# Performance work log

Measured on AMD Instinct MI355X. Metric: run time of the kernel, lower is better.

## Reference

```python
import jax, jax.numpy as jnp
import numpy as np

NEG_SLOPE = 0.01  # torch nn.LeakyReLU default


def setup_inputs() -> dict:
    key = jax.random.key(0)
    k1, k2, k3 = jax.random.split(key, 3)
    B, H, D, L = 4, 8, 64, 2048
    q = jax.random.normal(k1, (B, H, D, L), dtype=jnp.float32)
    k = jax.random.normal(k2, (B, H, D, L), dtype=jnp.float32)
    v = jax.random.normal(k3, (B, H, D, L), dtype=jnp.float32)
    return {"q": q, "k": k, "v": v}


def reference(q, k, v):
    # q, k, v: [B, H, D, L] (note: feature dim BEFORE length, as in the torch module)
    d_tensor = q.shape[2]
    scale = 1.0 / np.sqrt(d_tensor).astype(np.float32)
    # scores = LeakyReLU(q^T k / sqrt(d)) : [B, H, Lq, Lk]
    scores = jnp.einsum('bhdq,bhdk->bhqk', q, k) * scale
    scores = jax.nn.leaky_relu(scores, negative_slope=NEG_SLOPE)
    psi = jax.nn.softmax(scores, axis=-1)
    # out = (psi @ v^T)^T : [B, H, D, Lq]
    out = jnp.einsum('bhqk,bhdk->bhdq', psi, v)
    return out
```

## Files before the change

kernel.cpp:

```cpp
#include <hip/hip_runtime.h>
#include <math.h>

#define DD 64
#define LL 2048
#define TQ 128
#define TK 64
#define NTILES (LL / TK)
#define NTHREADS 512
#define NHEADS 32
#define QSCALE 0.18033688011112042f

typedef __bf16 bf16_t;
typedef __bf16 bf16x8 __attribute__((ext_vector_type(8)));
typedef float f32x16 __attribute__((ext_vector_type(16)));

struct __align__(16) SMemA {
  bf16_t Qs[TQ][72];
  bf16_t Ks[TK][72];
  bf16_t Vs[DD][72];
};
union __align__(16) SMemU {
  SMemA a;
  float Oe[TQ][65];
};

__global__ __launch_bounds__(256)
void prep_t(const float* __restrict__ src, bf16_t* __restrict__ dst, float scale) {
  __shared__ bf16_t tile[64][72];
  const int tid  = threadIdx.x;
  const int head = blockIdx.y;
  const int l0   = blockIdx.x * 64;
  const float* sp = src + (size_t)head * DD * LL;
  {
    int d  = tid >> 2;
    int lg = (tid & 3) * 16;
    const float* rp = sp + (size_t)d * LL + l0 + lg;
    for (int g = 0; g < 4; ++g) {
      float4 a = *(const float4*)(rp + 4 * g);
      tile[lg + 4 * g + 0][d] = (bf16_t)(a.x * scale);
      tile[lg + 4 * g + 1][d] = (bf16_t)(a.y * scale);
      tile[lg + 4 * g + 2][d] = (bf16_t)(a.z * scale);
      tile[lg + 4 * g + 3][d] = (bf16_t)(a.w * scale);
    }
  }
  __syncthreads();
  {
    int l  = tid & 63;
    int dh = (tid >> 6) * 16;
    bf16x8 r0 = *(const bf16x8*)&tile[l][dh];
    bf16x8 r1 = *(const bf16x8*)&tile[l][dh + 8];
    bf16_t* op = dst + ((size_t)head * LL + l0 + l) * DD + dh;
    *(bf16x8*)op = r0;
    *(bf16x8*)(op + 8) = r1;
  }
}

__global__ __launch_bounds__(256)
void prep_c(const float* __restrict__ src, bf16_t* __restrict__ dst) {
  size_t i = ((size_t)blockIdx.x * 256 + threadIdx.x) * 8;
  float4 a = *(const float4*)(src + i);
  float4 b = *(const float4*)(src + i + 4);
  bf16x8 p;
  p[0] = (bf16_t)a.x; p[1] = (bf16_t)a.y; p[2] = (bf16_t)a.z; p[3] = (bf16_t)a.w;
  p[4] = (bf16_t)b.x; p[5] = (bf16_t)b.y; p[6] = (bf16_t)b.z; p[7] = (bf16_t)b.w;
  *(bf16x8*)(dst + i) = p;
}

__global__ __launch_bounds__(NTHREADS, 4)
void attn_flash_bf16(const bf16_t* __restrict__ Qt, const bf16_t* __restrict__ Kt,
                     const bf16_t* __restrict__ Vb, float* __restrict__ out) {
  __shared__ SMemU sm;
  __shared__ float rs1[TQ];
  const int tid  = threadIdx.x;
  const int w    = tid >> 6;
  const int lane = tid & 63;
  const int l31  = lane & 31;
  const int hh   = lane >> 5;
  const int strip = w & 3;
  const int half  = w >> 2;
  const int wbase = strip * 32;
  const int lkh   = half * 32;
  const int head = blockIdx.y;
  const int q0   = blockIdx.x * TQ;
  const bf16_t* qp = Qt + (size_t)head * LL * DD;
  const bf16_t* kp = Kt + (size_t)head * LL * DD;
  const bf16_t* vp = Vb + (size_t)head * DD * LL;

  {
    int lq  = tid & 127;
    int d0q = (tid >> 7) * 16;
    const bf16_t* src = qp + (size_t)(q0 + lq) * DD + d0q;
    bf16x8 a0 = *(const bf16x8*)src;
    bf16x8 a1 = *(const bf16x8*)(src + 8);
    *(bf16x8*)&sm.a.Qs[lq][d0q] = a0;
    *(bf16x8*)&sm.a.Qs[lq][d0q + 8] = a1;
  }

  const int klk = tid & 63;
  const int kd0 = (tid >> 6) * 8;
  const int vd  = tid >> 3;
  const int vc8 = (tid & 7) * 8;

  bf16x8 kreg = *(const bf16x8*)(kp + (size_t)klk * DD + kd0);
  bf16x8 vreg = *(const bf16x8*)(vp + (size_t)vd * LL + vc8);

  __syncthreads();
  bf16x8 bq[4];
  for (int kk = 0; kk < 4; ++kk)
    bq[kk] = *(const bf16x8*)&sm.a.Qs[wbase + l31][kk * 16 + 8 * hh];

  f32x16 oacc[2];
  for (int dt = 0; dt < 2; ++dt)
    for (int r = 0; r < 16; ++r) oacc[dt][r] = 0.f;
  float rsum = 0.f;

  for (int t = 0; t < NTILES; ++t) {
    __syncthreads();
    *(bf16x8*)&sm.a.Ks[klk][kd0] = kreg;
    *(bf16x8*)&sm.a.Vs[vd][vc8]  = vreg;
    __syncthreads();

    if (t + 1 < NTILES) {
      const int lk0n = (t + 1) * TK;
      kreg = *(const bf16x8*)(kp + (size_t)(lk0n + klk) * DD + kd0);
      vreg = *(const bf16x8*)(vp + (size_t)vd * LL + lk0n + vc8);
    }

    f32x16 st;
    for (int r = 0; r < 16; ++r) st[r] = 0.f;
    for (int kk = 0; kk < 4; ++kk) {
      bf16x8 ak = *(const bf16x8*)&sm.a.Ks[lkh + l31][kk * 16 + 8 * hh];
      st = __builtin_amdgcn_mfma_f32_32x32x16_bf16(ak, bq[kk], st, 0, 0, 0);
    }

    unsigned pb[8];
    for (int r = 0; r < 16; ++r) {
      float s = st[r];
      s = fmaxf(s, 0.01f * s);
      float p = __builtin_amdgcn_exp2f(s);
      rsum += p;
      st[r] = p;
    }
    for (int qq = 0; qq < 8; ++qq) {
      union { bf16_t b[2]; unsigned u; } pk;
      pk.b[0] = (bf16_t)st[2 * qq];
      pk.b[1] = (bf16_t)st[2 * qq + 1];
      pb[qq] = pk.u;
    }

    for (int kk2 = 0; kk2 < 2; ++kk2) {
      unsigned l0 = pb[4 * kk2 + 0], l1 = pb[4 * kk2 + 1];
      unsigned l2 = pb[4 * kk2 + 2], l3 = pb[4 * kk2 + 3];
      unsigned s0 = hh ? l0 : l2;
      unsigned s1 = hh ? l1 : l3;
      unsigned f0 = (unsigned)__shfl_xor((int)s0, 32);
      unsigned f1 = (unsigned)__shfl_xor((int)s1, 32);
      union { unsigned u[4]; bf16x8 v; } ap;
      ap.u[0] = hh ? f0 : l0;
      ap.u[1] = hh ? f1 : l1;
      ap.u[2] = hh ? l2 : f0;
      ap.u[3] = hh ? l3 : f1;
      const int lkb = lkh + kk2 * 16 + 8 * hh;
      for (int dt = 0; dt < 2; ++dt) {
        bf16x8 bv = *(const bf16x8*)&sm.a.Vs[dt * 32 + l31][lkb];
        oacc[dt] = __builtin_amdgcn_mfma_f32_32x32x16_bf16(ap.v, bv, oacc[dt], 0, 0, 0);
      }
    }
  }

  float rtot = rsum + __shfl_xor(rsum, 32);
  __syncthreads();
  if (half == 1) {
    rs1[wbase + l31] = rtot;
    for (int r = 0; r < 16; ++r) {
      int row = (r & 3) + 8 * (r >> 2) + 4 * hh;
      for (int dt = 0; dt < 2; ++dt)
        sm.Oe[wbase + row][dt * 32 + l31] = oacc[dt][r];
    }
  }
  __syncthreads();
  if (half == 0) {
    float tot = rtot + rs1[wbase + l31];
    rs1[wbase + l31] = 1.0f / tot;
    float inv[16];
    for (int r = 0; r < 16; ++r) {
      int row = (r & 3) + 8 * (r >> 2) + 4 * hh;
      inv[r] = rs1[wbase + row];
    }
    for (int r = 0; r < 16; ++r) {
      int row = (r & 3) + 8 * (r >> 2) + 4 * hh;
      for (int dt = 0; dt < 2; ++dt) {
        int col = dt * 32 + l31;
        sm.Oe[wbase + row][col] = (oacc[dt][r] + sm.Oe[wbase + row][col]) * inv[r];
      }
    }
  }
  __syncthreads();
  float* op = out + (size_t)head * DD * LL + q0;
  for (int i = 0; i < 16; ++i) {
    int idx = tid + NTHREADS * i;
    int d   = idx >> 7;
    int lq  = idx & 127;
    op[(size_t)d * LL + lq] = sm.Oe[lq][d];
  }
}

__global__ __launch_bounds__(NTHREADS, 4)
void attn_flash_fb(const float* __restrict__ q, const float* __restrict__ k,
                   const float* __restrict__ v, float* __restrict__ out) {
  __shared__ SMemU sm;
  __shared__ float rs1[TQ];
  const int tid  = threadIdx.x;
  const int w    = tid >> 6;
  const int lane = tid & 63;
  const int l31  = lane & 31;
  const int hh   = lane >> 5;
  const int strip = w & 3;
  const int half  = w >> 2;
  const int wbase = strip * 32;
  const int lkh   = half * 32;
  const int head = blockIdx.y;
  const int q0   = blockIdx.x * TQ;
  const size_t hoff = (size_t)head * DD * LL;
  const float* qp = q + hoff;
  const float* kp = k + hoff;
  const float* vp = v + hoff;
  {
    int lq  = tid & 127;
    int d0q = (tid >> 7) * 16;
    const float* src = qp + q0 + lq;
    for (int g = 0; g < 2; ++g) {
      bf16x8 pk;
      for (int j = 0; j < 8; ++j)
        pk[j] = (bf16_t)(src[(size_t)(d0q + g * 8 + j) * LL] * QSCALE);
      *(bf16x8*)&sm.a.Qs[lq][d0q + g * 8] = pk;
    }
  }
  const int klk = tid & 63;
  const int kd0 = (tid >> 6) * 8;
  const int vd  = tid >> 3;
  const int vc8 = (tid & 7) * 8;
  float  kreg[8];
  float4 vreg[2];
  {
    const float* ks = kp + klk;
    for (int j = 0; j < 8; ++j) kreg[j] = ks[(size_t)(kd0 + j) * LL];
    vreg[0] = *(const float4*)(vp + (size_t)vd * LL + vc8);
    vreg[1] = *(const float4*)(vp + (size_t)vd * LL + vc8 + 4);
  }
  __syncthreads();
  bf16x8 bq[4];
  for (int kk = 0; kk < 4; ++kk)
    bq[kk] = *(const bf16x8*)&sm.a.Qs[wbase + l31][kk * 16 + 8 * hh];
  f32x16 oacc[2];
  for (int dt = 0; dt < 2; ++dt)
    for (int r = 0; r < 16; ++r) oacc[dt][r] = 0.f;
  float rsum = 0.f;
  for (int t = 0; t < NTILES; ++t) {
    __syncthreads();
    {
      bf16x8 pk;
      for (int j = 0; j < 8; ++j) pk[j] = (bf16_t)kreg[j];
      *(bf16x8*)&sm.a.Ks[klk][kd0] = pk;
      bf16x8 pv;
      pv[0] = (bf16_t)vreg[0].x; pv[1] = (bf16_t)vreg[0].y;
      pv[2] = (bf16_t)vreg[0].z; pv[3] = (bf16_t)vreg[0].w;
      pv[4] = (bf16_t)vreg[1].x; pv[5] = (bf16_t)vreg[1].y;
      pv[6] = (bf16_t)vreg[1].z; pv[7] = (bf16_t)vreg[1].w;
      *(bf16x8*)&sm.a.Vs[vd][vc8] = pv;
    }
    __syncthreads();
    if (t + 1 < NTILES) {
      const int lk0n = (t + 1) * TK;
      const float* ks = kp + lk0n + klk;
      for (int j = 0; j < 8; ++j) kreg[j] = ks[(size_t)(kd0 + j) * LL];
      vreg[0] = *(const float4*)(vp + (size_t)vd * LL + lk0n + vc8);
      vreg[1] = *(const float4*)(vp + (size_t)vd * LL + lk0n + vc8 + 4);
    }
    f32x16 st;
    for (int r = 0; r < 16; ++r) st[r] = 0.f;
    for (int kk = 0; kk < 4; ++kk) {
      bf16x8 ak = *(const bf16x8*)&sm.a.Ks[lkh + l31][kk * 16 + 8 * hh];
      st = __builtin_amdgcn_mfma_f32_32x32x16_bf16(ak, bq[kk], st, 0, 0, 0);
    }
    unsigned pb[8];
    for (int r = 0; r < 16; ++r) {
      float s = st[r];
      s = fmaxf(s, 0.01f * s);
      float p = __builtin_amdgcn_exp2f(s);
      rsum += p;
      st[r] = p;
    }
    for (int qq = 0; qq < 8; ++qq) {
      union { bf16_t b[2]; unsigned u; } pk;
      pk.b[0] = (bf16_t)st[2 * qq];
      pk.b[1] = (bf16_t)st[2 * qq + 1];
      pb[qq] = pk.u;
    }
    for (int kk2 = 0; kk2 < 2; ++kk2) {
      unsigned l0 = pb[4 * kk2 + 0], l1 = pb[4 * kk2 + 1];
      unsigned l2 = pb[4 * kk2 + 2], l3 = pb[4 * kk2 + 3];
      unsigned s0 = hh ? l0 : l2;
      unsigned s1 = hh ? l1 : l3;
      unsigned f0 = (unsigned)__shfl_xor((int)s0, 32);
      unsigned f1 = (unsigned)__shfl_xor((int)s1, 32);
      union { unsigned u[4]; bf16x8 v; } ap;
      ap.u[0] = hh ? f0 : l0;
      ap.u[1] = hh ? f1 : l1;
      ap.u[2] = hh ? l2 : f0;
      ap.u[3] = hh ? l3 : f1;
      const int lkb = lkh + kk2 * 16 + 8 * hh;
      for (int dt = 0; dt < 2; ++dt) {
        bf16x8 bv = *(const bf16x8*)&sm.a.Vs[dt * 32 + l31][lkb];
        oacc[dt] = __builtin_amdgcn_mfma_f32_32x32x16_bf16(ap.v, bv, oacc[dt], 0, 0, 0);
      }
    }
  }
  float rtot = rsum + __shfl_xor(rsum, 32);
  __syncthreads();
  if (half == 1) {
    rs1[wbase + l31] = rtot;
    for (int r = 0; r < 16; ++r) {
      int row = (r & 3) + 8 * (r >> 2) + 4 * hh;
      for (int dt = 0; dt < 2; ++dt)
        sm.Oe[wbase + row][dt * 32 + l31] = oacc[dt][r];
    }
  }
  __syncthreads();
  if (half == 0) {
    float tot = rtot + rs1[wbase + l31];
    rs1[wbase + l31] = 1.0f / tot;
    float inv[16];
    for (int r = 0; r < 16; ++r) {
      int row = (r & 3) + 8 * (r >> 2) + 4 * hh;
      inv[r] = rs1[wbase + row];
    }
    for (int r = 0; r < 16; ++r) {
      int row = (r & 3) + 8 * (r >> 2) + 4 * hh;
      for (int dt = 0; dt < 2; ++dt) {
        int col = dt * 32 + l31;
        sm.Oe[wbase + row][col] = (oacc[dt][r] + sm.Oe[wbase + row][col]) * inv[r];
      }
    }
  }
  __syncthreads();
  float* op = out + hoff + q0;
  for (int i = 0; i < 16; ++i) {
    int idx = tid + NTHREADS * i;
    int d   = idx >> 7;
    int lq  = idx & 127;
    op[(size_t)d * LL + lq] = sm.Oe[lq][d];
  }
}

extern "C" void kernel_launch(void* const* d_in, const int* in_sizes, int n_in,
                              void* d_out, int out_size, void* d_ws, size_t ws_size,
                              hipStream_t stream) {
  const float* q = (const float*)d_in[0];
  const float* k = (const float*)d_in[1];
  const float* v = (const float*)d_in[2];
  float* out = (float*)d_out;
  const size_t tsz = (size_t)NHEADS * LL * DD;
  const size_t need = 3 * tsz * sizeof(bf16_t);
  dim3 grid(LL / TQ, NHEADS);
  if (ws_size >= need) {
    bf16_t* Qt = (bf16_t*)d_ws;
    bf16_t* Kt = Qt + tsz;
    bf16_t* Vb = Kt + tsz;
    dim3 pg(LL / 64, NHEADS);
    prep_t<<<pg, 256, 0, stream>>>(q, Qt, QSCALE);
    prep_t<<<pg, 256, 0, stream>>>(k, Kt, 1.0f);
    prep_c<<<(unsigned)(tsz / (256 * 8)), 256, 0, stream>>>(v, Vb);
    attn_flash_bf16<<<grid, NTHREADS, 0, stream>>>(Qt, Kt, Vb, out);
  } else {
    attn_flash_fb<<<grid, NTHREADS, 0, stream>>>(q, k, v, out);
  }
}
```

Baseline: 155.4 us.

## Retile attention to 64-query by 128-key blocks, fuse prep kernels, load Q directly

The main kernel now handles 64 queries per block with 128-key tiles, splitting the key tile across four wave groups and reducing their partial outputs and row sums through two shared-memory buffers. The three preprocessing launches become one kernel that converts K (transposed) and V to bf16, and Q is converted and scaled inside the attention kernel, so the Q workspace pass goes away. This cuts launch count and global traffic and doubles the grid for better occupancy. In exchange, K and V are read twice as often from L2 and the final reduction gets more complex.

```diff
diff --git a/kernel.cpp b/kernel.cpp
--- a/kernel.cpp
+++ b/kernel.cpp
@@ -3,106 +3,107 @@
 
 #define DD 64
 #define LL 2048
-#define TQ 128
-#define TK 64
+#define NHEADS 32
+#define NTHREADS 512
+#define TQ 64
+#define TK 128
 #define NTILES (LL / TK)
-#define NTHREADS 512
-#define NHEADS 32
+#define FTQ 128
+#define FTK 64
+#define FNTILES (LL / FTK)
 #define QSCALE 0.18033688011112042f
 
 typedef __bf16 bf16_t;
 typedef __bf16 bf16x8 __attribute__((ext_vector_type(8)));
 typedef float f32x16 __attribute__((ext_vector_type(16)));
 
-struct __align__(16) SMemA {
+struct __align__(16) SMemM {
   bf16_t Qs[TQ][72];
   bf16_t Ks[TK][72];
+  bf16_t Vs[DD][136];
+};
+struct __align__(16) SMemME {
+  float Oe1[TQ][65];
+  float Oe2[TQ][65];
+};
+union __align__(16) SMemMU { SMemM a; SMemME e; };
+
+struct __align__(16) SMemF {
+  bf16_t Qs[FTQ][72];
+  bf16_t Ks[FTK][72];
   bf16_t Vs[DD][72];
 };
-union __align__(16) SMemU {
-  SMemA a;
-  float Oe[TQ][65];
-};
+union __align__(16) SMemFU { SMemF a; float Oe[FTQ][65]; };
 
 __global__ __launch_bounds__(256)
-void prep_t(const float* __restrict__ src, bf16_t* __restrict__ dst, float scale) {
-  __shared__ bf16_t tile[64][72];
-  const int tid  = threadIdx.x;
-  const int head = blockIdx.y;
-  const int l0   = blockIdx.x * 64;
-  const float* sp = src + (size_t)head * DD * LL;
-  {
-    int d  = tid >> 2;
-    int lg = (tid & 3) * 16;
-    const float* rp = sp + (size_t)d * LL + l0 + lg;
-    for (int g = 0; g < 4; ++g) {
-      float4 a = *(const float4*)(rp + 4 * g);
-      tile[lg + 4 * g + 0][d] = (bf16_t)(a.x * scale);
-      tile[lg + 4 * g + 1][d] = (bf16_t)(a.y * scale);
-      tile[lg + 4 * g + 2][d] = (bf16_t)(a.z * scale);
-      tile[lg + 4 * g + 3][d] = (bf16_t)(a.w * scale);
-    }
-  }
-  __syncthreads();
-  {
-    int l  = tid & 63;
-    int dh = (tid >> 6) * 16;
-    bf16x8 r0 = *(const bf16x8*)&tile[l][dh];
-    bf16x8 r1 = *(const bf16x8*)&tile[l][dh + 8];
-    bf16_t* op = dst + ((size_t)head * LL + l0 + l) * DD + dh;
-    *(bf16x8*)op = r0;
-    *(bf16x8*)(op + 8) = r1;
+void prep(const float* __restrict__ k, const float* __restrict__ v,
+          bf16_t* __restrict__ Kt, bf16_t* __restrict__ Vb) {
+  const int bid = blockIdx.x;
+  const int tid = threadIdx.x;
+  if (bid < 1024) {
+    const int head = bid >> 5;
+    const int l0   = (bid & 31) * 64;
+    const float* sp = k + (size_t)head * DD * LL;
+    bf16_t* dp = Kt + ((size_t)head * LL + l0) * DD;
+    const int lk = tid & 63;
+    const int dg = (tid >> 6) * 8;
+    for (int rep = 0; rep < 2; ++rep) {
+      const int d0 = dg + rep * 32;
+      bf16x8 pk;
+      for (int j = 0; j < 8; ++j)
+        pk[j] = (bf16_t)sp[(size_t)(d0 + j) * LL + l0 + lk];
+      *(bf16x8*)(dp + (size_t)lk * DD + d0) = pk;
+    }
+  } else {
+    size_t i = ((size_t)(bid - 1024) * 256 + tid) * 8;
+    float4 a = *(const float4*)(v + i);
+    float4 b = *(const float4*)(v + i + 4);
+    bf16x8 p;
+    p[0] = (bf16_t)a.x; p[1] = (bf16_t)a.y; p[2] = (bf16_t)a.z; p[3] = (bf16_t)a.w;
+    p[4] = (bf16_t)b.x; p[5] = (bf16_t)b.y; p[6] = (bf16_t)b.z; p[7] = (bf16_t)b.w;
+    *(bf16x8*)(Vb + i) = p;
   }
 }
 
-__global__ __launch_bounds__(256)
-void prep_c(const float* __restrict__ src, bf16_t* __restrict__ dst) {
-  size_t i = ((size_t)blockIdx.x * 256 + threadIdx.x) * 8;
-  float4 a = *(const float4*)(src + i);
-  float4 b = *(const float4*)(src + i + 4);
-  bf16x8 p;
-  p[0] = (bf16_t)a.x; p[1] = (bf16_t)a.y; p[2] = (bf16_t)a.z; p[3] = (bf16_t)a.w;
-  p[4] = (bf16_t)b.x; p[5] = (bf16_t)b.y; p[6] = (bf16_t)b.z; p[7] = (bf16_t)b.w;
-  *(bf16x8*)(dst + i) = p;
-}
-
 __global__ __launch_bounds__(NTHREADS, 4)
-void attn_flash_bf16(const bf16_t* __restrict__ Qt, const bf16_t* __restrict__ Kt,
-                     const bf16_t* __restrict__ Vb, float* __restrict__ out) {
-  __shared__ SMemU sm;
-  __shared__ float rs1[TQ];
+void attn_main(const float* __restrict__ q, const bf16_t* __restrict__ Kt,
+               const bf16_t* __restrict__ Vb, float* __restrict__ out) {
+  __shared__ SMemMU sm;
+  __shared__ float rsA[TQ], rsB[TQ];
   const int tid  = threadIdx.x;
   const int w    = tid >> 6;
   const int lane = tid & 63;
   const int l31  = lane & 31;
   const int hh   = lane >> 5;
-  const int strip = w & 3;
-  const int half  = w >> 2;
+  const int strip = w & 1;
+  const int quart = w >> 1;
   const int wbase = strip * 32;
-  const int lkh   = half * 32;
+  const int lkh   = quart * 32;
   const int head = blockIdx.y;
   const int q0   = blockIdx.x * TQ;
-  const bf16_t* qp = Qt + (size_t)head * LL * DD;
+  const float*  qp = q  + (size_t)head * DD * LL;
   const bf16_t* kp = Kt + (size_t)head * LL * DD;
   const bf16_t* vp = Vb + (size_t)head * DD * LL;
 
   {
-    int lq  = tid & 127;
-    int d0q = (tid >> 7) * 16;
-    const bf16_t* src = qp + (size_t)(q0 + lq) * DD + d0q;
-    bf16x8 a0 = *(const bf16x8*)src;
-    bf16x8 a1 = *(const bf16x8*)(src + 8);
-    *(bf16x8*)&sm.a.Qs[lq][d0q] = a0;
-    *(bf16x8*)&sm.a.Qs[lq][d0q + 8] = a1;
-  }
-
-  const int klk = tid & 63;
-  const int kd0 = (tid >> 6) * 8;
-  const int vd  = tid >> 3;
-  const int vc8 = (tid & 7) * 8;
-
-  bf16x8 kreg = *(const bf16x8*)(kp + (size_t)klk * DD + kd0);
-  bf16x8 vreg = *(const bf16x8*)(vp + (size_t)vd * LL + vc8);
+    const int lq = tid & 63;
+    const int d0 = (tid >> 6) * 8;
+    const float* src = qp + q0 + lq;
+    bf16x8 pk;
+    for (int j = 0; j < 8; ++j)
+      pk[j] = (bf16_t)(src[(size_t)(d0 + j) * LL] * QSCALE);
+    *(bf16x8*)&sm.a.Qs[lq][d0] = pk;
+  }
+
+  const int klk  = tid & 127;
+  const int kd0  = (tid >> 7) * 16;
+  const int vd   = tid >> 3;
+  const int vc16 = (tid & 7) * 16;
+
+  bf16x8 kr0 = *(const bf16x8*)(kp + (size_t)klk * DD + kd0);
+  bf16x8 kr1 = *(const bf16x8*)(kp + (size_t)klk * DD + kd0 + 8);
+  bf16x8 vr0 = *(const bf16x8*)(vp + (size_t)vd * LL + vc16);
+  bf16x8 vr1 = *(const bf16x8*)(vp + (size_t)vd * LL + vc16 + 8);
 
   __syncthreads();
   bf16x8 bq[4];
@@ -116,14 +117,18 @@
 
   for (int t = 0; t < NTILES; ++t) {
     __syncthreads();
-    *(bf16x8*)&sm.a.Ks[klk][kd0] = kreg;
-    *(bf16x8*)&sm.a.Vs[vd][vc8]  = vreg;
+    *(bf16x8*)&sm.a.Ks[klk][kd0]      = kr0;
+    *(bf16x8*)&sm.a.Ks[klk][kd0 + 8]  = kr1;
+    *(bf16x8*)&sm.a.Vs[vd][vc16]      = vr0;
+    *(bf16x8*)&sm.a.Vs[vd][vc16 + 8]  = vr1;
     __syncthreads();
 
     if (t + 1 < NTILES) {
       const int lk0n = (t + 1) * TK;
-      kreg = *(const bf16x8*)(kp + (size_t)(lk0n + klk) * DD + kd0);
-      vreg = *(const bf16x8*)(vp + (size_t)vd * LL + lk0n + vc8);
+      kr0 = *(const bf16x8*)(kp + (size_t)(lk0n + klk) * DD + kd0);
+      kr1 = *(const bf16x8*)(kp + (size_t)(lk0n + klk) * DD + kd0 + 8);
+      vr0 = *(const bf16x8*)(vp + (size_t)vd * LL + lk0n + vc16);
+      vr1 = *(const bf16x8*)(vp + (size_t)vd * LL + lk0n + vc16 + 8);
     }
 
     f32x16 st;
@@ -170,46 +175,54 @@
 
   float rtot = rsum + __shfl_xor(rsum, 32);
   __syncthreads();
-  if (half == 1) {
-    rs1[wbase + l31] = rtot;
-    for (int r = 0; r < 16; ++r) {
-      int row = (r & 3) + 8 * (r >> 2) + 4 * hh;
-      for (int dt = 0; dt < 2; ++dt)
-        sm.Oe[wbase + row][dt * 32 + l31] = oacc[dt][r];
-    }
-  }
-  __syncthreads();
-  if (half == 0) {
-    float tot = rtot + rs1[wbase + l31];
-    rs1[wbase + l31] = 1.0f / tot;
-    float inv[16];
-    for (int r = 0; r < 16; ++r) {
-      int row = (r & 3) + 8 * (r >> 2) + 4 * hh;
-      inv[r] = rs1[wbase + row];
-    }
-    for (int r = 0; r < 16; ++r) {
-      int row = (r & 3) + 8 * (r >> 2) + 4 * hh;
-      for (int dt = 0; dt < 2; ++dt) {
-        int col = dt * 32 + l31;
-        sm.Oe[wbase + row][col] = (oacc[dt][r] + sm.Oe[wbase + row][col]) * inv[r];
-      }
-    }
-  }
+  if (quart == 0) {
+    rsA[wbase + l31] = rtot;
+    for (int r = 0; r < 16; ++r) {
+      int row = (r & 3) + 8 * (r >> 2) + 4 * hh;
+      for (int dt = 0; dt < 2; ++dt)
+        sm.e.Oe1[wbase + row][dt * 32 + l31] = oacc[dt][r];
+    }
+  } else if (quart == 2) {
+    rsB[wbase + l31] = rtot;
+    for (int r = 0; r < 16; ++r) {
+      int row = (r & 3) + 8 * (r >> 2) + 4 * hh;
+      for (int dt = 0; dt < 2; ++dt)
+        sm.e.Oe2[wbase + row][dt * 32 + l31] = oacc[dt][r];
+    }
+  }
+  __syncthreads();
+  if (quart == 1) {
+    rsA[wbase + l31] += rtot;
+    for (int r = 0; r < 16; ++r) {
+      int row = (r & 3) + 8 * (r >> 2) + 4 * hh;
+      for (int dt = 0; dt < 2; ++dt)
+        sm.e.Oe1[wbase + row][dt * 32 + l31] += oacc[dt][r];
+    }
+  } else if (quart == 3) {
+    rsB[wbase + l31] += rtot;
+    for (int r = 0; r < 16; ++r) {
+      int row = (r & 3) + 8 * (r >> 2) + 4 * hh;
+      for (int dt = 0; dt < 2; ++dt)
+        sm.e.Oe2[wbase + row][dt * 32 + l31] += oacc[dt][r];
+    }
+  }
+  __syncthreads();
+  if (tid < TQ) rsA[tid] = 1.0f / (rsA[tid] + rsB[tid]);
   __syncthreads();
   float* op = out + (size_t)head * DD * LL + q0;
-  for (int i = 0; i < 16; ++i) {
+  for (int i = 0; i < 8; ++i) {
     int idx = tid + NTHREADS * i;
-    int d   = idx >> 7;
-    int lq  = idx & 127;
-    op[(size_t)d * LL + lq] = sm.Oe[lq][d];
+    int d   = idx >> 6;
+    int lq  = idx & 63;
+    op[(size_t)d * LL + lq] = (sm.e.Oe1[lq][d] + sm.e.Oe2[lq][d]) * rsA[lq];
   }
 }
 
 __global__ __launch_bounds__(NTHREADS, 4)
 void attn_flash_fb(const float* __restrict__ q, const float* __restrict__ k,
                    const float* __restrict__ v, float* __restrict__ out) {
-  __shared__ SMemU sm;
-  __shared__ float rs1[TQ];
+  __shared__ SMemFU sm;
+  __shared__ float rs1[FTQ];
   const int tid  = threadIdx.x;
   const int w    = tid >> 6;
   const int lane = tid & 63;
@@ -220,7 +233,7 @@
   const int wbase = strip * 32;
   const int lkh   = half * 32;
   const int head = blockIdx.y;
-  const int q0   = blockIdx.x * TQ;
+  const int q0   = blockIdx.x * FTQ;
   const size_t hoff = (size_t)head * DD * LL;
   const float* qp = q + hoff;
   const float* kp = k + hoff;
@@ -256,7 +269,7 @@
   for (int dt = 0; dt < 2; ++dt)
     for (int r = 0; r < 16; ++r) oacc[dt][r] = 0.f;
   float rsum = 0.f;
-  for (int t = 0; t < NTILES; ++t) {
+  for (int t = 0; t < FNTILES; ++t) {
     __syncthreads();
     {
       bf16x8 pk;
@@ -270,8 +283,8 @@
       *(bf16x8*)&sm.a.Vs[vd][vc8] = pv;
     }
     __syncthreads();
-    if (t + 1 < NTILES) {
-      const int lk0n = (t + 1) * TK;
+    if (t + 1 < FNTILES) {
+      const int lk0n = (t + 1) * FTK;
       const float* ks = kp + lk0n + klk;
       for (int j = 0; j < 8; ++j) kreg[j] = ks[(size_t)(kd0 + j) * LL];
       vreg[0] = *(const float4*)(vp + (size_t)vd * LL + lk0n + vc8);
@@ -360,19 +373,16 @@
   const float* k = (const float*)d_in[1];
   const float* v = (const float*)d_in[2];
   float* out = (float*)d_out;
-  const size_t tsz = (size_t)NHEADS * LL * DD;
-  const size_t need = 3 * tsz * sizeof(bf16_t);
-  dim3 grid(LL / TQ, NHEADS);
+  const size_t tsz  = (size_t)NHEADS * LL * DD;
+  const size_t need = 2 * tsz * sizeof(bf16_t);
   if (ws_size >= need) {
-    bf16_t* Qt = (bf16_t*)d_ws;
-    bf16_t* Kt = Qt + tsz;
+    bf16_t* Kt = (bf16_t*)d_ws;
     bf16_t* Vb = Kt + tsz;
-    dim3 pg(LL / 64, NHEADS);
-    prep_t<<<pg, 256, 0, stream>>>(q, Qt, QSCALE);
-    prep_t<<<pg, 256, 0, stream>>>(k, Kt, 1.0f);
-    prep_c<<<(unsigned)(tsz / (256 * 8)), 256, 0, stream>>>(v, Vb);
-    attn_flash_bf16<<<grid, NTHREADS, 0, stream>>>(Qt, Kt, Vb, out);
+    prep<<<1024 + 2048, 256, 0, stream>>>(k, v, Kt, Vb);
+    dim3 grid(LL / TQ, NHEADS);
+    attn_main<<<grid, NTHREADS, 0, stream>>>(q, Kt, Vb, out);
   } else {
+    dim3 grid(LL / FTQ, NHEADS);
     attn_flash_fb<<<grid, NTHREADS, 0, stream>>>(q, k, v, out);
   }
 }
```

Result: no change. 155.4 us (+0.0%).
